# Kernel optimization log

Measured on AMD Instinct MI355X. Metric: run time of the kernel, lower is better.

Reference implementation:

```python
import jax, jax.numpy as jnp
import numpy as np
from jax import lax

TWN_THRESHOLD_FACTOR = 0.05
BN_EPS = 1e-5


@jax.custom_vjp
def _ternary_quant(w, t):
    return (w > t).astype(w.dtype) - (w < -t).astype(w.dtype)

def _tq_fwd(w, t):
    mask = (w > t) | (w < -t)
    return _ternary_quant(w, t), mask

def _tq_bwd(mask, g):
    return (g * mask.astype(g.dtype), jnp.zeros((), g.dtype))

_ternary_quant.defvjp(_tq_fwd, _tq_bwd)


def quantize(w):
    # threshold is detached in the original (weight.detach().abs().max())
    t = TWN_THRESHOLD_FACTOR * jnp.max(jnp.abs(lax.stop_gradient(w)))
    return _ternary_quant(w, t)


def conv2d(x, w, b):
    # x: [N,C,H,W], w: [O,I,K,K], valid conv, stride 1
    y = lax.conv_general_dilated(x, w, (1, 1), 'VALID',
                                 dimension_numbers=('NCHW', 'OIHW', 'NCHW'))
    return y + b[None, :, None, None]


def maxpool2(x):
    return lax.reduce_window(x, -jnp.inf, lax.max,
                             (1, 1, 2, 2), (1, 1, 2, 2), 'VALID')


def bn2d(x, g, b):
    # training-mode batch norm over (N,H,W), biased variance
    m = jnp.mean(x, (0, 2, 3), keepdims=True)
    v = jnp.mean(jnp.square(x - m), (0, 2, 3), keepdims=True)
    return (x - m) * lax.rsqrt(v + BN_EPS) * g[None, :, None, None] + b[None, :, None, None]


def bn1d(x, g, b):
    m = jnp.mean(x, 0, keepdims=True)
    v = jnp.mean(jnp.square(x - m), 0, keepdims=True)
    return (x - m) * lax.rsqrt(v + BN_EPS) * g[None, :] + b[None, :]


def setup_inputs() -> dict:
    key = jax.random.key(0)
    ks = jax.random.split(key, 12)
    N = 4096
    inp = {
        'x': jax.random.normal(ks[0], (N, 1, 28, 28), jnp.float32),
        'w1': jax.random.normal(ks[1], (32, 1, 5, 5), jnp.float32) * 0.2,
        'b1': jnp.zeros((32,), jnp.float32),
        'g1': jnp.ones((32,), jnp.float32),
        'be1': jnp.zeros((32,), jnp.float32),
        'w2': jax.random.normal(ks[2], (64, 32, 5, 5), jnp.float32) * 0.05,
        'b2': jnp.zeros((64,), jnp.float32),
        'g2': jnp.ones((64,), jnp.float32),
        'be2': jnp.zeros((64,), jnp.float32),
        'wf1': jax.random.normal(ks[3], (512, 1024), jnp.float32) * 0.03,
        'bf1': jnp.zeros((512,), jnp.float32),
        'g3': jnp.ones((512,), jnp.float32),
        'be3': jnp.zeros((512,), jnp.float32),
        'wf2': jax.random.normal(ks[4], (10, 512), jnp.float32) * 0.04,
        'bf2': jnp.zeros((10,), jnp.float32),
    }
    return inp


def reference(x, w1, b1, g1, be1, w2, b2, g2, be2, wf1, bf1, g3, be3, wf2, bf2):
    h = jax.nn.relu(bn2d(conv2d(x, quantize(w1), b1), g1, be1))     # [N,32,24,24]
    h = maxpool2(h)                                                  # [N,32,12,12]
    h = jax.nn.relu(bn2d(conv2d(h, quantize(w2), b2), g2, be2))     # [N,64,8,8]
    h = maxpool2(h)                                                  # [N,64,4,4]
    h = h.reshape(h.shape[0], -1)                                    # [N,1024]
    h = jax.nn.relu(bn1d(h @ quantize(wf1).T + bf1, g3, be3))       # [N,512]
    return h @ quantize(wf2).T + bf2                                 # [N,10]
```

## Files before the change

kernel.cpp:

```cpp
#include <hip/hip_runtime.h>

#define TID ((int)threadIdx.x)
typedef unsigned short u16;
typedef short short8 __attribute__((ext_vector_type(8)));
typedef float f32x4 __attribute__((ext_vector_type(4)));

__device__ __forceinline__ u16 f2b(float f) {
    unsigned int x = __float_as_uint(f);
    return (u16)((x + 0x7fffu + ((x >> 16) & 1u)) >> 16);
}
__device__ __forceinline__ float b2f(u16 u) {
    return __uint_as_float(((unsigned int)u) << 16);
}
__device__ __forceinline__ unsigned int cvt_pk(float lo, float hi) {
    unsigned int r;
    asm("v_cvt_pk_bf16_f32 %0, %1, %2" : "=v"(r) : "v"(lo), "v"(hi));
    return r;
}
__device__ __forceinline__ float xmax32(float w) {
    unsigned int a = __float_as_uint(w), b = a;
    asm("v_permlane32_swap_b32 %0, %1" : "+v"(a), "+v"(b));
    return fmaxf(__uint_as_float(a), __uint_as_float(b));
}

static constexpr size_t OFF_QW1   = 0;
static constexpr size_t OFF_QWF2  = 3200;
static constexpr size_t OFF_TMAX  = 23680;
static constexpr size_t OFF_SUM1C = 23808;
static constexpr size_t OFF_SSQ1C = 24832;
static constexpr size_t OFF_SUM2  = 25856, OFF_SSQ2 = 26112;
static constexpr size_t OFF_SUM3  = 26368, OFF_SSQ3 = 28416;
static constexpr size_t STATS_BEG = 23680, STATS_END = 30464;
static constexpr size_t OFF_QW2C  = 30720;
static constexpr size_t OFF_QWF1C = 133120;
static constexpr size_t OFF_Y1P   = 1181696;
static constexpr size_t OFF_H2P   = 38930432;
static constexpr size_t OFF_Y3    = 47319040;

__global__ __launch_bounds__(256) void absmax_k(const float* w1, const float* w2,
                                                const float* wf1, const float* wf2,
                                                unsigned int* tmaxbits) {
    int bid = blockIdx.x;
    int b, lb, nb; const float* src; long n;
    if (bid < 1)        { b = 0; src = w1;  n = 800;    lb = bid;       nb = 1;   }
    else if (bid < 9)   { b = 1; src = w2;  n = 51200;  lb = bid - 1;   nb = 8;   }
    else if (bid < 265) { b = 2; src = wf1; n = 524288; lb = bid - 9;   nb = 256; }
    else                { b = 3; src = wf2; n = 5120;   lb = bid - 265; nb = 1;   }
    float m = 0.f;
    for (long i = (long)lb * 256 + TID; i < n; i += (long)nb * 256)
        m = fmaxf(m, fabsf(src[i]));
    __shared__ float red[256];
    red[TID] = m; __syncthreads();
    for (int s = 128; s > 0; s >>= 1) {
        if (TID < s) red[TID] = fmaxf(red[TID], red[TID + s]);
        __syncthreads();
    }
    if (TID == 0) atomicMax(&tmaxbits[b], __float_as_uint(red[0]));
}

__global__ __launch_bounds__(256) void quant_all_k(const float* w1, const float* w2,
                                                   const float* wf1, const float* wf2,
                                                   float* qw1, u16* qw2c, u16* qwf1c,
                                                   float* qwf2, const unsigned int* tmax) {
    int bid = blockIdx.x;
    if (bid < 4) {
        int i = bid * 256 + TID; if (i >= 800) return;
        float t = 0.05f * __uint_as_float(tmax[0]);
        float v = w1[i];
        qw1[i] = (v > t) ? 1.f : ((v < -t) ? -1.f : 0.f);
    } else if (bid < 204) {
        int i = (bid - 4) * 256 + TID;
        float t = 0.05f * __uint_as_float(tmax[1]);
        int ic = i & 31, oc = (i >> 5) & 63, sh = i >> 11;
        float v = w2[(oc * 32 + ic) * 25 + sh];
        qw2c[i] = (v > t) ? (u16)0x3F80 : ((v < -t) ? (u16)0xBF80 : (u16)0);
    } else if (bid < 2252) {
        int i = (bid - 204) * 256 + TID;
        float t = 0.05f * __uint_as_float(tmax[2]);
        float v = wf1[i];
        qwf1c[i] = (v > t) ? (u16)0x3F80 : ((v < -t) ? (u16)0xBF80 : (u16)0);
    } else {
        int i = (bid - 2252) * 256 + TID;
        float t = 0.05f * __uint_as_float(tmax[3]);
        float v = wf2[i];
        qwf2[i] = (v > t) ? 1.f : ((v < -t) ? -1.f : 0.f);
    }
}

__global__ __launch_bounds__(256) void conv1_fused_k(const float* __restrict__ x,
                                                     const float* __restrict__ qw1,
                                                     u16* __restrict__ y1p,
                                                     float* sum1c, float* ssq1c) {
    __shared__ __align__(16) u16 xs[16 * 1096];
    int gid = blockIdx.x;
    int sg = gid >> 2, ph = (gid >> 1) & 1, pch = gid & 1;
    int l = TID & 63, w = TID >> 6;
    int lm = l & 15, q = l >> 4;

    #pragma unroll
    for (int i = 0; i < 9; i++) {
        int idx = TID + i * 256;
        if (idx < 2192) reinterpret_cast<uint4*>(xs)[idx] = make_uint4(0, 0, 0, 0);
    }

    short8 B1[2], B2[2];
    #pragma unroll
    for (int c = 0; c < 2; c++) {
        union { short8 s; u16 h[8]; } b1, b2;
        int ch = c * 16 + lm;
        #pragma unroll
        for (int j = 0; j < 8; j++) {
            float v1 = 0.f, v2 = 0.f;
            if (j < 5) {
                v1 = qw1[ch * 25 + q * 5 + j];
                v2 = qw1[ch * 25 + 20 + j];
            }
            b1.h[j] = f2b(v1);
            b2.h[j] = (q == 0) ? f2b(v2) : (u16)0;
        }
        B1[c] = b1.s; B2[c] = b2.s;
    }
    __syncthreads();

    #pragma unroll
    for (int k = 0; k < 7; k++) {
        int i = TID + k * 256;
        int smp = i / 112, rem = i % 112;
        int row = rem / 7, c4 = (rem % 7) * 4;
        float4 v = *reinterpret_cast<const float4*>(
            x + (size_t)(sg * 16 + smp) * 784 + (12 * ph + row) * 28 + c4);
        unsigned int r0 = cvt_pk(v.x, v.y), r1 = cvt_pk(v.z, v.w);
        uint2 pk; pk.x = r0; pk.y = r1;
        *reinterpret_cast<uint2*>(xs + smp * 1096 + row * 32 + c4) = pk;
        u16 h[4] = {(u16)r0, (u16)(r0 >> 16), (u16)r1, (u16)(r1 >> 16)};
        u16* b1p = xs + smp * 1096 + 548 + row * 32;
        #pragma unroll
        for (int e = 0; e < 4; e++) {
            int c = c4 + e;
            if (c >= 1) b1p[c - 1] = h[e];
        }
    }
    __syncthreads();

    float s0 = 0.f, s1 = 0.f, q0 = 0.f, q1 = 0.f;
    int laneoff = lm * 1096;
    #pragma unroll 1
    for (int e = 0; e < 9; e++) {
        int pp = w * 9 + e;
        int prl = pp / 6, pcl = pp - prl * 6;
        f32x4 pm0 = {-3.0e38f, -3.0e38f, -3.0e38f, -3.0e38f};
        f32x4 pm1 = pm0;
        #pragma unroll
        for (int dyx = 0; dyx < 4; dyx++) {
            int dy = dyx >> 1, dx = dyx & 1;
            int oyl = 2 * prl + dy;
            int ox = 2 * (pch * 6 + pcl) + dx;
            int r = ox & 1, cb = ox - r;
            const u16* p1 = xs + laneoff + r * 548 + (oyl + q) * 32 + cb;
            const u16* p2 = xs + laneoff + r * 548 + (oyl + 4) * 32 + cb;
            union { short8 s; unsigned int u[4]; } a1, a2;
            #pragma unroll
            for (int t = 0; t < 4; t++) {
                a1.u[t] = *reinterpret_cast<const unsigned int*>(p1 + 2 * t);
                a2.u[t] = *reinterpret_cast<const unsigned int*>(p2 + 2 * t);
            }
            f32x4 d0 = {0.f, 0.f, 0.f, 0.f};
            d0 = __builtin_amdgcn_mfma_f32_16x16x32_bf16(a1.s, B1[0], d0, 0, 0, 0);
            d0 = __builtin_amdgcn_mfma_f32_16x16x32_bf16(a2.s, B2[0], d0, 0, 0, 0);
            f32x4 d1 = {0.f, 0.f, 0.f, 0.f};
            d1 = __builtin_amdgcn_mfma_f32_16x16x32_bf16(a1.s, B1[1], d1, 0, 0, 0);
            d1 = __builtin_amdgcn_mfma_f32_16x16x32_bf16(a2.s, B2[1], d1, 0, 0, 0);
            #pragma unroll
            for (int i = 0; i < 4; i++) {
                float v = d0[i]; s0 += v; q0 = fmaf(v, v, q0);
                float u = d1[i]; s1 += u; q1 = fmaf(u, u, q1);
            }
            pm0 = __builtin_elementwise_max(pm0, d0);
            pm1 = __builtin_elementwise_max(pm1, d1);
        }
        int ppg = (ph * 6 + prl) * 12 + (pch * 6 + pcl);
        #pragma unroll
        for (int i = 0; i < 4; i++) {
            size_t nb = (size_t)(sg * 16 + 4 * q + i) * 4608 + ppg * 32;
            unsigned int r = cvt_pk(pm0[i], pm1[i]);
            y1p[nb + lm]      = (u16)r;
            y1p[nb + 16 + lm] = (u16)(r >> 16);
        }
    }
    s0 += __shfl_xor(s0, 16); s0 += __shfl_xor(s0, 32);
    s1 += __shfl_xor(s1, 16); s1 += __shfl_xor(s1, 32);
    q0 += __shfl_xor(q0, 16); q0 += __shfl_xor(q0, 32);
    q1 += __shfl_xor(q1, 16); q1 += __shfl_xor(q1, 32);
    if (l < 16) {
        int slot = (blockIdx.x & 7) * 32;
        atomicAdd(&sum1c[slot + l], s0);
        atomicAdd(&sum1c[slot + 16 + l], s1);
        atomicAdd(&ssq1c[slot + l], q0);
        atomicAdd(&ssq1c[slot + 16 + l], q1);
    }
}

__global__ __launch_bounds__(256) void conv2_k(const u16* __restrict__ y1p,
                                               const u16* __restrict__ qw2c,
                                               u16* __restrict__ h2pre,
                                               const float* sum1c, const float* ssq1c,
                                               const float* g1, const float* be1,
                                               float* sum, float* ssq) {
    __shared__ float4 hsm4[1176];
    __shared__ float scs[32], shs[32];
    char* hsraw = (char*)hsm4;
    int n0 = blockIdx.x * 8;
    int l = TID & 63, wv = TID >> 6;
    int oc0 = wv * 16;
    int lm = l & 15, lr = (l >> 3) & 1, ox = l & 7, bq = l >> 4;
    if (TID < 32) {
        float s = 0.f, q = 0.f;
        #pragma unroll
        for (int r = 0; r < 8; r++) { s += sum1c[r * 32 + TID]; q += ssq1c[r * 32 + TID]; }
        float m = s * (1.f / 2359296.f);
        float v = q * (1.f / 2359296.f) - m * m;
        float sc = g1[TID] / sqrtf(v + 1e-5f);
        scs[TID] = sc; shs[TID] = be1[TID] - m * sc;
    }
    __syncthreads();
    float scR[8], shR[8];
    {
        int b = TID & 3;
        #pragma unroll
        for (int j = 0; j < 8; j++) { scR[j] = scs[b * 8 + j]; shR[j] = shs[b * 8 + j]; }
    }
    short8 bw[25];
    #pragma unroll
    for (int sh = 0; sh < 25; sh++)
        bw[sh] = *reinterpret_cast<const short8*>(qw2c + ((size_t)sh * 64 + oc0 + lm) * 32 + bq * 8);
    int xy[5];
    #pragma unroll
    for (int kx = 0; kx < 5; kx++) {
        int xx = ox + kx;
        xy[kx] = lr * 784 + xx * 64 + (((bq + (xx >> 1)) & 3) * 16);
    }
    float sacc = 0.f, s2acc = 0.f;
    {
        const uint4* src = reinterpret_cast<const uint4*>(y1p + (size_t)n0 * 4608);
        #pragma unroll
        for (int k = 0; k < 3; k++) {
            if (k < 2 || TID < 64) {
                int i = TID + k * 256;
                int pix = i >> 2, b = i & 3;
                int y = pix / 12, xx = pix - y * 12;
                union { uint4 v; u16 u[8]; } in;
                in.v = src[i];
                float f[8];
                #pragma unroll
                for (int j = 0; j < 8; j++)
                    f[j] = fmaxf(fmaf(b2f(in.u[j]), scR[j], shR[j]), 0.f);
                uint4 o = make_uint4(cvt_pk(f[0], f[1]), cvt_pk(f[2], f[3]),
                                     cvt_pk(f[4], f[5]), cvt_pk(f[6], f[7]));
                *reinterpret_cast<uint4*>(hsraw + y * 784 + xx * 64 + (((b + (xx >> 1)) & 3) * 16)) = o;
            }
        }
    }
    #pragma unroll 1
    for (int s = 0; s < 8; s++) {
        __syncthreads();
        uint4 pf0 = {}, pf1 = {}, pf2 = {};
        if (s < 7) {
            const uint4* src = reinterpret_cast<const uint4*>(y1p + (size_t)(n0 + s + 1) * 4608);
            pf0 = src[TID];
            pf1 = src[TID + 256];
            if (TID < 64) pf2 = src[TID + 512];
        }
        const char* hb = hsraw + (s & 1) * 9408;
        f32x4 acc[4] = {{0.f,0.f,0.f,0.f},{0.f,0.f,0.f,0.f},{0.f,0.f,0.f,0.f},{0.f,0.f,0.f,0.f}};
        #pragma unroll
        for (int R = 0; R <= 10; R++) {
            short8 a[5];
            #pragma unroll
            for (int kx = 0; kx < 5; kx++)
                a[kx] = *reinterpret_cast<const short8*>(hb + xy[kx] + R * 784);
            #pragma unroll
            for (int mt = 0; mt < 4; mt++) {
                int ky = R - 2 * mt;
                if (ky < 0 || ky > 4) continue;
                #pragma unroll
                for (int kx = 0; kx < 5; kx++)
                    acc[mt] = __builtin_amdgcn_mfma_f32_16x16x32_bf16(a[kx], bw[ky * 5 + kx], acc[mt], 0, 0, 0);
            }
        }
        int n = n0 + s;
        u16* hp = h2pre + (size_t)n * 1024 + (oc0 + lm) * 16;
        #pragma unroll
        for (int mt = 0; mt < 4; mt++) {
            float v0 = acc[mt][0], v1 = acc[mt][1], v2 = acc[mt][2], v3 = acc[mt][3];
            sacc += v0 + v1 + v2 + v3;
            s2acc += v0 * v0 + v1 * v1 + v2 * v2 + v3 * v3;
            float w0 = fmaxf(v0, v1), w1 = fmaxf(v2, v3);
            float p0 = xmax32(w0);
            float p1 = xmax32(w1);
            if (bq < 2) {
                *reinterpret_cast<unsigned int*>(hp + mt * 4 + bq * 2) = cvt_pk(p0, p1);
            }
        }
        if (s < 7) {
            char* dst = hsraw + ((s + 1) & 1) * 9408;
            #pragma unroll
            for (int k = 0; k < 3; k++) {
                if (k < 2 || TID < 64) {
                    int i = TID + k * 256;
                    int pix = i >> 2, b = i & 3;
                    int y = pix / 12, xx = pix - y * 12;
                    union { uint4 v; u16 u[8]; } in;
                    in.v = (k == 0) ? pf0 : ((k == 1) ? pf1 : pf2);
                    float f[8];
                    #pragma unroll
                    for (int j = 0; j < 8; j++)
                        f[j] = fmaxf(fmaf(b2f(in.u[j]), scR[j], shR[j]), 0.f);
                    uint4 o = make_uint4(cvt_pk(f[0], f[1]), cvt_pk(f[2], f[3]),
                                         cvt_pk(f[4], f[5]), cvt_pk(f[6], f[7]));
                    *reinterpret_cast<uint4*>(dst + y * 784 + xx * 64 + (((b + (xx >> 1)) & 3) * 16)) = o;
                }
            }
        }
    }
    sacc  += __shfl_xor(sacc, 16);  sacc  += __shfl_xor(sacc, 32);
    s2acc += __shfl_xor(s2acc, 16); s2acc += __shfl_xor(s2acc, 32);
    if (l < 16) { atomicAdd(&sum[oc0 + l], sacc); atomicAdd(&ssq[oc0 + l], s2acc); }
}

__global__ __launch_bounds__(256) void fc1_k(const u16* __restrict__ h2pre,
                                             const u16* __restrict__ qwf1c,
                                             const float* sum2, const float* ssq2,
                                             const float* g2, const float* be2,
                                             float* __restrict__ y3T,
                                             float* sum3, float* ssq3) {
    __shared__ float4 Asm[576], Bsm[576];
    __shared__ float sc2s[64], sh2s[64];
    u16* AsU = (u16*)Asm; u16* BsU = (u16*)Bsm;
    int m0 = blockIdx.x * 64, j0 = blockIdx.y * 64;
    int l = TID & 63, wv = TID >> 6;
    int lm = l & 15, q = l >> 4;
    int r0 = TID >> 3, c0 = TID & 7;
    if (TID < 64) {
        float m = sum2[TID] * (1.f / 262144.f);
        float v = ssq2[TID] * (1.f / 262144.f) - m * m;
        float s = g2[TID] / sqrtf(v + 1e-5f);
        sc2s[TID] = s; sh2s[TID] = be2[TID] - m * s;
    }
    __syncthreads();
    f32x4 acc[4] = {{0.f,0.f,0.f,0.f},{0.f,0.f,0.f,0.f},{0.f,0.f,0.f,0.f},{0.f,0.f,0.f,0.f}};
    #pragma unroll 1
    for (int kc = 0; kc < 16; kc++) {
        int kk = kc * 64;
        if (kc) __syncthreads();
        int oc = (kk + c0 * 8) >> 4;
        float sc = sc2s[oc], sh = sh2s[oc];
        #pragma unroll
        for (int i = 0; i < 2; i++) {
            int r = i * 32 + r0;
            union { float4 v; u16 h[8]; } in;
            in.v = *reinterpret_cast<const float4*>(h2pre + (size_t)(m0 + r) * 1024 + kk + c0 * 8);
            float f[8];
            #pragma unroll
            for (int e = 0; e < 8; e++)
                f[e] = fmaxf(fmaf(b2f(in.h[e]), sc, sh), 0.f);
            uint4 o = make_uint4(cvt_pk(f[0], f[1]), cvt_pk(f[2], f[3]),
                                 cvt_pk(f[4], f[5]), cvt_pk(f[6], f[7]));
            *reinterpret_cast<uint4*>(AsU + r * 72 + c0 * 8) = o;
            *reinterpret_cast<float4*>(BsU + r * 72 + c0 * 8) =
                *reinterpret_cast<const float4*>(qwf1c + (size_t)(j0 + r) * 1024 + kk + c0 * 8);
        }
        __syncthreads();
        #pragma unroll
        for (int half = 0; half < 2; half++) {
            short8 b = *reinterpret_cast<const short8*>(BsU + (wv * 16 + lm) * 72 + half * 32 + q * 8);
            #pragma unroll
            for (int mt = 0; mt < 4; mt++) {
                short8 a = *reinterpret_cast<const short8*>(AsU + (mt * 16 + lm) * 72 + half * 32 + q * 8);
                acc[mt] = __builtin_amdgcn_mfma_f32_16x16x32_bf16(a, b, acc[mt], 0, 0, 0);
            }
        }
    }
    float s = 0.f, s2 = 0.f;
    #pragma unroll
    for (int mt = 0; mt < 4; mt++) {
        *reinterpret_cast<f32x4*>(y3T + (size_t)(j0 + wv * 16 + lm) * 4096 + m0 + mt * 16 + q * 4) = acc[mt];
        #pragma unroll
        for (int i = 0; i < 4; i++) { float v = acc[mt][i]; s += v; s2 = fmaf(v, v, s2); }
    }
    s  += __shfl_xor(s, 16);  s  += __shfl_xor(s, 32);
    s2 += __shfl_xor(s2, 16); s2 += __shfl_xor(s2, 32);
    if (l < 16) {
        atomicAdd(&sum3[j0 + wv * 16 + l], s);
        atomicAdd(&ssq3[j0 + wv * 16 + l], s2);
    }
}

__global__ __launch_bounds__(256) void fc2_k(const float* __restrict__ y3T,
                                             const float* sum3, const float* ssq3,
                                             const float* g3, const float* be3,
                                             const float* __restrict__ qwf2,
                                             const float* bf2, float* __restrict__ out) {
    __shared__ float wlds[5120];
    __shared__ float part[15][160];
    __shared__ float sc3s[512], sh3s[512];
    for (int i = TID; i < 5120; i += 256) wlds[i] = qwf2[i];
    for (int k = TID; k < 512; k += 256) {
        float m = sum3[k] * (1.f / 4096.f);
        float v = ssq3[k] * (1.f / 4096.f) - m * m;
        float s = g3[k] / sqrtf(v + 1e-5f);
        sc3s[k] = s; sh3s[k] = be3[k] - m * s;
    }
    __syncthreads();
    int nl = TID & 15, ks = TID >> 4;
    int n = blockIdx.x * 16 + nl;
    float acc[10] = {};
    for (int k = ks * 32; k < ks * 32 + 32; k++) {
        float v = fmaxf(y3T[(size_t)k * 4096 + n] * sc3s[k] + sh3s[k], 0.f);
        #pragma unroll
        for (int o = 0; o < 10; o++) acc[o] = fmaf(v, wlds[o * 512 + k], acc[o]);
    }
    if (ks > 0) {
        #pragma unroll
        for (int o = 0; o < 10; o++) part[ks - 1][o * 16 + nl] = acc[o];
    }
    __syncthreads();
    if (ks == 0) {
        #pragma unroll
        for (int o = 0; o < 10; o++) {
            float r = acc[o] + bf2[o];
            #pragma unroll
            for (int j = 0; j < 15; j++) r += part[j][o * 16 + nl];
            out[n * 10 + o] = r;
        }
    }
}

extern "C" void kernel_launch(void* const* d_in, const int* in_sizes, int n_in,
                              void* d_out, int out_size, void* d_ws, size_t ws_size,
                              hipStream_t stream) {
    char* wsb = (char*)d_ws;
    const float* x   = (const float*)d_in[0];
    const float* w1  = (const float*)d_in[1];
    const float* g1  = (const float*)d_in[3];
    const float* be1 = (const float*)d_in[4];
    const float* w2  = (const float*)d_in[5];
    const float* g2  = (const float*)d_in[7];
    const float* be2 = (const float*)d_in[8];
    const float* wf1 = (const float*)d_in[9];
    const float* g3  = (const float*)d_in[11];
    const float* be3 = (const float*)d_in[12];
    const float* wf2 = (const float*)d_in[13];
    const float* bf2 = (const float*)d_in[14];
    float* out = (float*)d_out;

    unsigned int* tmax = (unsigned int*)(wsb + OFF_TMAX);
    float* qw1   = (float*)(wsb + OFF_QW1);
    float* qwf2  = (float*)(wsb + OFF_QWF2);
    u16*   qw2c  = (u16*)(wsb + OFF_QW2C);
    u16*   qwf1c = (u16*)(wsb + OFF_QWF1C);
    u16*   y1p   = (u16*)(wsb + OFF_Y1P);
    u16*   h2pre = (u16*)(wsb + OFF_H2P);
    float* y3    = (float*)(wsb + OFF_Y3);

    float* sum1c = (float*)(wsb + OFF_SUM1C); float* ssq1c = (float*)(wsb + OFF_SSQ1C);
    float* sum2  = (float*)(wsb + OFF_SUM2);  float* ssq2  = (float*)(wsb + OFF_SSQ2);
    float* sum3  = (float*)(wsb + OFF_SUM3);  float* ssq3  = (float*)(wsb + OFF_SSQ3);

    hipMemsetAsync(wsb + STATS_BEG, 0, STATS_END - STATS_BEG, stream);

    absmax_k<<<266, 256, 0, stream>>>(w1, w2, wf1, wf2, tmax);
    quant_all_k<<<2272, 256, 0, stream>>>(w1, w2, wf1, wf2, qw1, qw2c, qwf1c, qwf2, tmax);

    conv1_fused_k<<<1024, 256, 0, stream>>>(x, qw1, y1p, sum1c, ssq1c);
    conv2_k<<<512, 256, 0, stream>>>(y1p, qw2c, h2pre, sum1c, ssq1c, g1, be1, sum2, ssq2);
    fc1_k<<<dim3(64, 8), 256, 0, stream>>>(h2pre, qwf1c, sum2, ssq2, g2, be2, y3, sum3, ssq3);
    fc2_k<<<256, 256, 0, stream>>>(y3, sum3, ssq3, g3, be3, qwf2, bf2, out);
}
```

Before: 208.0 us.

## Split conv2 block into two 256-thread groups each handling alternating images

conv2_k now launches 512 threads per block, forming two independent groups of four waves. Each group has its own double-buffered LDS tile and processes every other image of the block's eight, so each group runs four iterations instead of eight. This gives each block more waves to hide latency and halves the serial loop length per wave. In exchange it doubles LDS per block, and the shared __syncthreads now couples both groups.

Result: slower. 222.2 us (+6.8%).

```diff
diff --git a/kernel.cpp b/kernel.cpp
--- a/kernel.cpp
+++ b/kernel.cpp
@@ -200,19 +200,22 @@
     }
 }
 
-__global__ __launch_bounds__(256) void conv2_k(const u16* __restrict__ y1p,
+__global__ __launch_bounds__(512) void conv2_k(const u16* __restrict__ y1p,
                                                const u16* __restrict__ qw2c,
                                                u16* __restrict__ h2pre,
                                                const float* sum1c, const float* ssq1c,
                                                const float* g1, const float* be1,
                                                float* sum, float* ssq) {
-    __shared__ float4 hsm4[1176];
+    __shared__ float4 hsm4[2352];
     __shared__ float scs[32], shs[32];
     char* hsraw = (char*)hsm4;
     int n0 = blockIdx.x * 8;
     int l = TID & 63, wv = TID >> 6;
-    int oc0 = wv * 16;
+    int g = wv >> 2;
+    int lt = TID & 255;
+    int oc0 = (wv & 3) * 16;
     int lm = l & 15, lr = (l >> 3) & 1, ox = l & 7, bq = l >> 4;
+    char* bufA = hsraw + g * 18816;
     if (TID < 32) {
         float s = 0.f, q = 0.f;
         #pragma unroll
@@ -241,11 +244,11 @@
     }
     float sacc = 0.f, s2acc = 0.f;
     {
-        const uint4* src = reinterpret_cast<const uint4*>(y1p + (size_t)n0 * 4608);
+        const uint4* src = reinterpret_cast<const uint4*>(y1p + (size_t)(n0 + g) * 4608);
         #pragma unroll
         for (int k = 0; k < 3; k++) {
-            if (k < 2 || TID < 64) {
-                int i = TID + k * 256;
+            if (k < 2 || lt < 64) {
+                int i = lt + k * 256;
                 int pix = i >> 2, b = i & 3;
                 int y = pix / 12, xx = pix - y * 12;
                 union { uint4 v; u16 u[8]; } in;
@@ -256,21 +259,21 @@
                     f[j] = fmaxf(fmaf(b2f(in.u[j]), scR[j], shR[j]), 0.f);
                 uint4 o = make_uint4(cvt_pk(f[0], f[1]), cvt_pk(f[2], f[3]),
                                      cvt_pk(f[4], f[5]), cvt_pk(f[6], f[7]));
-                *reinterpret_cast<uint4*>(hsraw + y * 784 + xx * 64 + (((b + (xx >> 1)) & 3) * 16)) = o;
+                *reinterpret_cast<uint4*>(bufA + y * 784 + xx * 64 + (((b + (xx >> 1)) & 3) * 16)) = o;
             }
         }
     }
     #pragma unroll 1
-    for (int s = 0; s < 8; s++) {
+    for (int t = 0; t < 4; t++) {
         __syncthreads();
         uint4 pf0 = {}, pf1 = {}, pf2 = {};
-        if (s < 7) {
-            const uint4* src = reinterpret_cast<const uint4*>(y1p + (size_t)(n0 + s + 1) * 4608);
-            pf0 = src[TID];
-            pf1 = src[TID + 256];
-            if (TID < 64) pf2 = src[TID + 512];
-        }
-        const char* hb = hsraw + (s & 1) * 9408;
+        if (t < 3) {
+            const uint4* src = reinterpret_cast<const uint4*>(y1p + (size_t)(n0 + 2 * (t + 1) + g) * 4608);
+            pf0 = src[lt];
+            pf1 = src[lt + 256];
+            if (lt < 64) pf2 = src[lt + 512];
+        }
+        const char* hb = bufA + (t & 1) * 9408;
         f32x4 acc[4] = {{0.f,0.f,0.f,0.f},{0.f,0.f,0.f,0.f},{0.f,0.f,0.f,0.f},{0.f,0.f,0.f,0.f}};
         #pragma unroll
         for (int R = 0; R <= 10; R++) {
@@ -287,7 +290,7 @@
                     acc[mt] = __builtin_amdgcn_mfma_f32_16x16x32_bf16(a[kx], bw[ky * 5 + kx], acc[mt], 0, 0, 0);
             }
         }
-        int n = n0 + s;
+        int n = n0 + 2 * t + g;
         u16* hp = h2pre + (size_t)n * 1024 + (oc0 + lm) * 16;
         #pragma unroll
         for (int mt = 0; mt < 4; mt++) {
@@ -301,12 +304,12 @@
                 *reinterpret_cast<unsigned int*>(hp + mt * 4 + bq * 2) = cvt_pk(p0, p1);
             }
         }
-        if (s < 7) {
-            char* dst = hsraw + ((s + 1) & 1) * 9408;
+        if (t < 3) {
+            char* dst = bufA + ((t + 1) & 1) * 9408;
             #pragma unroll
             for (int k = 0; k < 3; k++) {
-                if (k < 2 || TID < 64) {
-                    int i = TID + k * 256;
+                if (k < 2 || lt < 64) {
+                    int i = lt + k * 256;
                     int pix = i >> 2, b = i & 3;
                     int y = pix / 12, xx = pix - y * 12;
                     union { uint4 v; u16 u[8]; } in;
@@ -472,7 +475,7 @@
     quant_all_k<<<2272, 256, 0, stream>>>(w1, w2, wf1, wf2, qw1, qw2c, qwf1c, qwf2, tmax);
 
     conv1_fused_k<<<1024, 256, 0, stream>>>(x, qw1, y1p, sum1c, ssq1c);
-    conv2_k<<<512, 256, 0, stream>>>(y1p, qw2c, h2pre, sum1c, ssq1c, g1, be1, sum2, ssq2);
+    conv2_k<<<512, 512, 0, stream>>>(y1p, qw2c, h2pre, sum1c, ssq1c, g1, be1, sum2, ssq2);
     fc1_k<<<dim3(64, 8), 256, 0, stream>>>(h2pre, qwf1c, sum2, ssq2, g2, be2, y3, sum3, ssq3);
     fc2_k<<<256, 256, 0, stream>>>(y3, sum3, ssq3, g3, be3, qwf2, bf2, out);
 }
```
